# Kernel tuning notes

Measured on AMD Instinct MI355X. Metric: run time of the kernel, lower is better.

## Reference

```python
import jax, jax.numpy as jnp
import numpy as np

EPS = 1e-3  # BatchNorm eps (eval mode: running_mean=0, running_var=1)
GRID_D, GRID_H, GRID_W, GRID_C = 10, 400, 352, 128


def bn_last(x, g, b):
    # BatchNorm1d eval over last (channel) axis
    return x * (g / jnp.sqrt(1.0 + EPS)) + b


def bn_ch(x, g, b):
    # BatchNorm3d eval, channel axis 1 of NCDHW
    s = (g / jnp.sqrt(1.0 + EPS)).reshape(1, -1, 1, 1, 1)
    return x * s + b.reshape(1, -1, 1, 1, 1)


def vfe_layer(x, W, g, b):
    # x: [N, T, Cin] -> [N, T, 2*units]
    h = jnp.einsum('ntc,uc->ntu', x, W)
    h = jax.nn.relu(bn_last(h, g, b))
    agg = jnp.max(h, axis=1, keepdims=True)          # [N,1,units]
    return jnp.concatenate([h, jnp.broadcast_to(agg, h.shape)], axis=2)


def pad3(x, p):
    # torch ConstantPad3d order: (Wl, Wr, Hl, Hr, Dl, Dr); x is NCDHW
    return jnp.pad(x, ((0, 0), (0, 0), (p[4], p[5]), (p[2], p[3]), (p[0], p[1])))


def conv3d(x, w, stride):
    return jax.lax.conv_general_dilated(
        x, w, window_strides=stride, padding='VALID',
        dimension_numbers=('NCDHW', 'OIDHW', 'NCDHW'))


def setup_inputs() -> dict:
    key = jax.random.key(0)
    ks = jax.random.split(key, 12)
    N, T = 20000, 35
    features = jax.random.normal(ks[0], (N, T, 4), jnp.float32)
    num_voxels = jax.random.randint(ks[1], (N,), 1, T + 1, jnp.int32)
    cb = jnp.zeros((N, 1), jnp.int32)
    cd = jax.random.randint(ks[2], (N, 1), 0, GRID_D, jnp.int32)
    ch = jax.random.randint(ks[3], (N, 1), 0, GRID_H, jnp.int32)
    cw = jax.random.randint(ks[4], (N, 1), 0, GRID_W, jnp.int32)
    coors = jnp.concatenate([cb, cd, ch, cw], axis=1)

    def lin(k, o, i):
        return jax.random.normal(k, (o, i), jnp.float32) / np.sqrt(i)

    def cw3(k, o, i):
        return jax.random.normal(k, (o, i, 3, 3, 3), jnp.float32) / np.sqrt(i * 27)

    return {
        'features': features, 'num_voxels': num_voxels, 'coors': coors, 'batch_size': 1,
        'w_vfe1': lin(ks[5], 16, 7), 'g_vfe1': jnp.ones(16), 'b_vfe1': jnp.zeros(16),
        'w_vfe2': lin(ks[6], 64, 32), 'g_vfe2': jnp.ones(64), 'b_vfe2': jnp.zeros(64),
        'w_lin': lin(ks[7], 128, 128), 'g_lin': jnp.ones(128), 'b_lin': jnp.zeros(128),
        'w_c1': cw3(ks[8], 64, 128), 'g_c1': jnp.ones(64), 'b_c1': jnp.zeros(64),
        'w_c2': cw3(ks[9], 64, 64), 'g_c2': jnp.ones(64), 'b_c2': jnp.zeros(64),
        'w_c3': cw3(ks[10], 64, 64), 'g_c3': jnp.ones(64), 'b_c3': jnp.zeros(64),
    }


def reference(features, num_voxels, coors, batch_size,
              w_vfe1, g_vfe1, b_vfe1, w_vfe2, g_vfe2, b_vfe2,
              w_lin, g_lin, b_lin,
              w_c1, g_c1, b_c1, w_c2, g_c2, b_c2, w_c3, g_c3, b_c3):
    # --- VoxelFeatureExtractor ---
    nv = num_voxels.astype(features.dtype)[:, None, None]
    points_mean = features[:, :, :3].sum(axis=1, keepdims=True) / nv
    rel = features[:, :, :3] - points_mean
    f = jnp.concatenate([features, rel], axis=-1)                 # [N,T,7]
    T = f.shape[1]
    mask = (jnp.arange(T)[None, :] < num_voxels[:, None]).astype(f.dtype)[..., None]
    x = vfe_layer(f, w_vfe1, g_vfe1, b_vfe1) * mask               # [N,T,32]
    x = vfe_layer(x, w_vfe2, g_vfe2, b_vfe2) * mask               # [N,T,128]
    x = jnp.einsum('ntc,uc->ntu', x, w_lin)
    x = jax.nn.relu(bn_last(x, g_lin, b_lin)) * mask
    voxelwise = jnp.max(x, axis=1)                                # [N,128]

    # --- MiddleExtractor: scatter_nd + 3D convs ---
    grid = jnp.zeros((batch_size, GRID_D, GRID_H, GRID_W, GRID_C), f.dtype)
    grid = grid.at[coors[:, 0], coors[:, 1], coors[:, 2], coors[:, 3]].set(voxelwise)
    r = grid.transpose(0, 4, 1, 2, 3)                             # NCDHW [1,128,10,400,352]
    r = pad3(r, (1, 1, 1, 1, 1, 1))
    r = jax.nn.relu(bn_ch(conv3d(r, w_c1, (2, 1, 1)), g_c1, b_c1))  # [1,64,5,400,352]
    r = pad3(r, (1, 1, 1, 1, 0, 0))
    r = jax.nn.relu(bn_ch(conv3d(r, w_c2, (1, 1, 1)), g_c2, b_c2))  # [1,64,3,400,352]
    r = pad3(r, (1, 1, 1, 1, 1, 1))
    r = jax.nn.relu(bn_ch(conv3d(r, w_c3, (2, 1, 1)), g_c3, b_c3))  # [1,64,2,400,352]
    Nb, C, D, H, W = r.shape
    return r.reshape(Nb, C * D, H, W)                             # [1,128,400,352]
```

## Files before the change

kernel.cpp:

```cpp
#include <hip/hip_runtime.h>
#include <hip/hip_bf16.h>

#define BNC 0.99950037f
#define GH 400
#define GW 352

typedef __bf16 bf16_t;
typedef __bf16 bf16x8 __attribute__((ext_vector_type(8)));
typedef float f32x4 __attribute__((ext_vector_type(4)));

__global__ void k_winner(const int* __restrict__ coors, int* __restrict__ winner, int N) {
    int i = blockIdx.x * 256 + threadIdx.x;
    if (i >= N) return;
    int d = coors[i*4+1], h = coors[i*4+2], w = coors[i*4+3];
    atomicMax(&winner[(d*GH + h)*GW + w], i);
}

__global__ void k_tr_w(const float* __restrict__ w, float* __restrict__ wt, int CI, int CO) {
    int idx = blockIdx.x * 256 + threadIdx.x;
    int total = 27 * CI * CO;
    if (idx >= total) return;
    int j   = idx & 3;
    int t1  = idx >> 2;
    int co  = t1 % CO;
    int t2  = t1 / CO;
    int ci4 = t2 % (CI/4);
    int tap = t2 / (CI/4);
    int ci  = ci4*4 + j;
    wt[idx] = w[(co*CI + ci)*27 + tap];
}

__global__ void k_tr_lin(const float* __restrict__ wl, float* __restrict__ WT) {
    int idx = blockIdx.x * 256 + threadIdx.x;
    if (idx >= 16384) return;
    int u = idx & 127, c = idx >> 7;
    WT[c*128 + u] = wl[u*128 + c];
}

__global__ void k_prep(const float* __restrict__ g, const float* __restrict__ b,
                       float* __restrict__ out) {
    int i = threadIdx.x;
    if (i < 64)       out[i] = g[i] * BNC;
    else if (i < 128) out[i] = b[i-64];
    else if (i < 192) out[i] = 1.f;
    else              out[i] = 0.f;
}

__global__ void k_packw(const float* __restrict__ w, bf16_t* __restrict__ wh,
                        bf16_t* __restrict__ wlo) {
    int i = blockIdx.x * 256 + threadIdx.x;
    if (i >= 13824) return;
    int lane = i & 63, ct = (i >> 6) & 3, s = i >> 8;
    int tap = s >> 1, h = s & 1;
    int kg = lane >> 4, wl = lane & 15;
    int co = ct*16 + wl;
    #pragma unroll
    for (int j = 0; j < 8; ++j) {
        int ci = h*32 + kg*8 + j;
        float v = w[(co*64 + ci)*27 + tap];
        bf16_t hi = (bf16_t)v;
        wh[(long)i*8 + j]  = hi;
        wlo[(long)i*8 + j] = (bf16_t)(v - (float)hi);
    }
}

__global__ __launch_bounds__(128) void k_vfe(
    const float* __restrict__ feats, const int* __restrict__ nvox,
    const float* __restrict__ w1, const float* __restrict__ g1g, const float* __restrict__ b1g,
    const float* __restrict__ w2g, const float* __restrict__ g2g, const float* __restrict__ b2g,
    const float* __restrict__ WT, const float* __restrict__ glg, const float* __restrict__ blg,
    float* __restrict__ voxelwise)
{
    __shared__ float F[35*8];
    __shared__ float W1s[16*8];
    __shared__ float SG1[16], SB1[16];
    __shared__ float X1[35*20];
    __shared__ float X2[35*68];
    __shared__ float RED[8*128];
    __shared__ float AGG1[16];
    __shared__ float AGG2[64];
    __shared__ float Y2B[64];
    __shared__ float YB[128];
    __shared__ float MEANS[3];

    int tid = threadIdx.x;
    int vox = blockIdx.x;
    int nv  = nvox[vox];

    const float* fsrc = feats + (long)vox * 140;
    for (int idx = tid; idx < 140; idx += 128) { int t = idx>>2, c = idx&3; F[t*8+c] = fsrc[idx]; }
    if (tid < 35) F[tid*8+7] = 0.f;
    if (tid < 112) { int u = tid/7, c = tid - u*7; W1s[u*8+c] = w1[tid]; }
    if (tid < 16)  { W1s[tid*8+7] = 0.f; SG1[tid] = g1g[tid]*BNC; SB1[tid] = b1g[tid]; }
    __syncthreads();

    if (tid < 3) {
        float s = 0.f;
        for (int t = 0; t < 35; ++t) s += F[t*8 + tid];
        MEANS[tid] = s / (float)nv;
    }
    __syncthreads();
    for (int idx = tid; idx < 105; idx += 128) { int t = idx/3, c = idx - t*3; F[t*8+4+c] = F[t*8+c] - MEANS[c]; }
    __syncthreads();

    {
        const float4* Ff4  = (const float4*)F;
        const float4* W1f4 = (const float4*)W1s;
        for (int idx = tid; idx < 560; idx += 128) {
            int t = idx >> 4, u = idx & 15;
            float4 a0 = Ff4[t*2], a1 = Ff4[t*2+1];
            float4 b0 = W1f4[u*2], b1v = W1f4[u*2+1];
            float a = a0.x*b0.x + a0.y*b0.y + a0.z*b0.z + a0.w*b0.w
                    + a1.x*b1v.x + a1.y*b1v.y + a1.z*b1v.z + a1.w*b1v.w;
            X1[t*20+u] = fmaxf(a*SG1[u] + SB1[u], 0.f);
        }
    }
    __syncthreads();
    if (tid < 16) {
        float m = 0.f;
        for (int t = 0; t < 35; ++t) m = fmaxf(m, X1[t*20+tid]);
        AGG1[tid] = m;
    }
    __syncthreads();
    if (tid < 64) {
        const float4* wsrc = (const float4*)(w2g + tid*32 + 16);
        const float4* A1f4 = (const float4*)AGG1;
        float a = 0.f;
        #pragma unroll
        for (int q = 0; q < 4; ++q) {
            float4 w4 = wsrc[q], x4 = A1f4[q];
            a += x4.x*w4.x + x4.y*w4.y + x4.z*w4.z + x4.w*w4.w;
        }
        Y2B[tid] = a;
    }
    __syncthreads();

    {
        int u = tid & 63, tg = tid >> 6;
        float w2r[16];
        const float4* wsrc = (const float4*)(w2g + u*32);
        #pragma unroll
        for (int q = 0; q < 4; ++q) {
            float4 w4 = wsrc[q];
            w2r[q*4] = w4.x; w2r[q*4+1] = w4.y; w2r[q*4+2] = w4.z; w2r[q*4+3] = w4.w;
        }
        float su = g2g[u]*BNC, bu = b2g[u];
        float yb2 = Y2B[u];
        float lm = (nv < 35) ? fmaxf(bu, 0.f) : 0.f;
        for (int t = tg; t < nv; t += 2) {
            const float4* xr = (const float4*)(X1 + t*20);
            float a = yb2;
            #pragma unroll
            for (int q = 0; q < 4; ++q) {
                float4 x4 = xr[q];
                a += x4.x*w2r[q*4] + x4.y*w2r[q*4+1] + x4.z*w2r[q*4+2] + x4.w*w2r[q*4+3];
            }
            float h = fmaxf(a*su + bu, 0.f);
            X2[t*68 + u] = h;
            lm = fmaxf(lm, h);
        }
        RED[tg*64 + u] = lm;
    }
    __syncthreads();
    if (tid < 64) AGG2[tid] = fmaxf(RED[tid], RED[64+tid]);
    __syncthreads();
    {
        float a = 0.f;
        for (int c = 0; c < 64; ++c) a = fmaf(AGG2[c], WT[(64 + c)*128 + tid], a);
        YB[tid] = a;
    }
    __syncthreads();

    {
        int ug = tid & 15, tg4 = tid >> 4;
        int u0 = ug * 8;
        int kmax = (nv > tg4) ? ((nv - tg4 + 7) >> 3) : 0;
        float acc[5][8];
        #pragma unroll
        for (int k = 0; k < 5; ++k)
            #pragma unroll
            for (int j = 0; j < 8; ++j) acc[k][j] = 0.f;

        const float4* X2f4 = (const float4*)X2;
        const float4* WTf4 = (const float4*)WT;
        for (int c4 = 0; c4 < 16; ++c4) {
            float4 wv[8];
            #pragma unroll
            for (int cc = 0; cc < 4; ++cc) {
                wv[cc*2]   = WTf4[(c4*4+cc)*32 + ug*2];
                wv[cc*2+1] = WTf4[(c4*4+cc)*32 + ug*2 + 1];
            }
            #pragma unroll
            for (int k = 0; k < 5; ++k) {
                if (k < kmax) {
                    int t = tg4 + (k << 3);
                    float4 x4 = X2f4[t*17 + c4];
                    #pragma unroll
                    for (int cc = 0; cc < 4; ++cc) {
                        float xs = (cc == 0) ? x4.x : (cc == 1) ? x4.y : (cc == 2) ? x4.z : x4.w;
                        acc[k][0] = fmaf(xs, wv[cc*2].x,   acc[k][0]);
                        acc[k][1] = fmaf(xs, wv[cc*2].y,   acc[k][1]);
                        acc[k][2] = fmaf(xs, wv[cc*2].z,   acc[k][2]);
                        acc[k][3] = fmaf(xs, wv[cc*2].w,   acc[k][3]);
                        acc[k][4] = fmaf(xs, wv[cc*2+1].x, acc[k][4]);
                        acc[k][5] = fmaf(xs, wv[cc*2+1].y, acc[k][5]);
                        acc[k][6] = fmaf(xs, wv[cc*2+1].z, acc[k][6]);
                        acc[k][7] = fmaf(xs, wv[cc*2+1].w, acc[k][7]);
                    }
                }
            }
        }
        float4 g0 = *(const float4*)(glg + u0), g1v = *(const float4*)(glg + u0 + 4);
        float4 b0 = *(const float4*)(blg + u0), b1v = *(const float4*)(blg + u0 + 4);
        float4 y0 = *(const float4*)(YB + u0),  y1v = *(const float4*)(YB + u0 + 4);
        float sg[8] = {g0.x*BNC, g0.y*BNC, g0.z*BNC, g0.w*BNC,
                       g1v.x*BNC, g1v.y*BNC, g1v.z*BNC, g1v.w*BNC};
        float sb[8] = {b0.x, b0.y, b0.z, b0.w, b1v.x, b1v.y, b1v.z, b1v.w};
        float yv[8] = {y0.x, y0.y, y0.z, y0.w, y1v.x, y1v.y, y1v.z, y1v.w};
        float m[8];
        #pragma unroll
        for (int j = 0; j < 8; ++j) m[j] = 0.f;
        #pragma unroll
        for (int k = 0; k < 5; ++k) {
            if (k < kmax) {
                #pragma unroll
                for (int j = 0; j < 8; ++j)
                    m[j] = fmaxf(m[j], fmaxf((acc[k][j] + yv[j])*sg[j] + sb[j], 0.f));
            }
        }
        #pragma unroll
        for (int j = 0; j < 8; ++j) RED[tg4*128 + u0 + j] = m[j];
    }
    __syncthreads();
    {
        float m = RED[tid];
        #pragma unroll
        for (int r = 1; r < 8; ++r) m = fmaxf(m, RED[r*128 + tid]);
        voxelwise[(long)vox*128 + tid] = m;
    }
}

__global__ __launch_bounds__(256) void k_gat1(
    const float4* __restrict__ voxf4, const int* __restrict__ winner,
    const float4* __restrict__ Wt1, float* __restrict__ accS,
    int h_lo, int AR)
{
    int r  = blockIdx.y;
    int oh = h_lo + r;
    if ((unsigned)oh >= (unsigned)GH) return;
    int doo = blockIdx.z;
    int w0  = blockIdx.x * 32;

    __shared__ int sList[306];
    __shared__ int sCnt;
    __shared__ float4 sF[32][32];

    int t = threadIdx.x;
    if (t == 0) sCnt = 0;
    __syncthreads();
    for (int idx = t; idx < 306; idx += 256) {
        int x = idx % 34, q = idx / 34;
        int kd = q / 3, kh = q - kd*3;
        int dp = doo*2 + kd - 1;
        int hp = oh + kh - 1;
        int wp = w0 - 1 + x;
        if ((unsigned)dp < 10u && (unsigned)hp < (unsigned)GH && (unsigned)wp < (unsigned)GW) {
            int v = winner[(dp*GH + hp)*GW + wp];
            if (v >= 0) {
                int p = atomicAdd(&sCnt, 1);
                sList[p] = (v << 10) | (kd << 8) | (kh << 6) | x;
            }
        }
    }
    __syncthreads();
    int cnt = sCnt;

    int co = t & 63, wv = t >> 6;
    int ibase = wv*8;
    float acc[8];
    #pragma unroll
    for (int i = 0; i < 8; ++i) acc[i] = 0.f;

    for (int c0 = 0; c0 < cnt; c0 += 32) {
        int nch = min(32, cnt - c0);
        __syncthreads();
        for (int idx = t; idx < nch*32; idx += 256) {
            int slot = idx >> 5, c = idx & 31;
            int widx = sList[c0 + slot] >> 10;
            sF[slot][c] = voxf4[(long)widx*32 + c];
        }
        __syncthreads();
        for (int e = 0; e < nch; ++e) {
            int ent = sList[c0 + e];
            int x = ent & 63, kh = (ent >> 6) & 3, kd = (ent >> 8) & 3;
            #pragma unroll
            for (int kw = 0; kw < 3; ++kw) {
                int i = x - kw;
                if (i >= ibase && i < ibase + 8) {
                    const float4* wb = Wt1 + (long)(kd*9 + kh*3 + kw)*2048 + co;
                    float a = 0.f;
                    #pragma unroll 4
                    for (int c4 = 0; c4 < 32; ++c4) {
                        float4 wq = wb[c4*64];
                        float4 f4 = sF[e][c4];
                        a += f4.x*wq.x + f4.y*wq.y + f4.z*wq.z + f4.w*wq.w;
                    }
                    int j = i - ibase;
                    #pragma unroll
                    for (int j8 = 0; j8 < 8; ++j8)
                        if (j8 == j) acc[j8] += a;
                }
            }
        }
    }

    long rowb = ((long)doo*AR + r)*GW + w0;
    #pragma unroll
    for (int i = 0; i < 8; ++i)
        accS[(rowb + ibase + i)*64 + co] = acc[i];
}

__global__ __launch_bounds__(256) void k_convm(
    const float* __restrict__ src, int src_h0, long src_dpitch,
    float* __restrict__ dst, int dst_h0, long sC, long sD, long sH, long sW,
    const bf16_t* __restrict__ wph, const bf16_t* __restrict__ wpl,
    const float* __restrict__ gact,
    const float* __restrict__ gout, const float* __restrict__ bout,
    int D_in, int d_stride, int d_pad, int y0)
{
    int oh = y0 + (int)blockIdx.y;
    if ((unsigned)oh >= (unsigned)GH) return;

    __shared__ __align__(16) char smem[17408];
    bf16_t* sAh = (bf16_t*)smem;
    bf16_t* sAl = (bf16_t*)(smem + 8448);
    float*  sOut = (float*)smem;

    int t = threadIdx.x;
    int lane = t & 63, wv = t >> 6;
    int wl = lane & 15, kg = lane >> 4;
    int mh = wv >> 1, cth = wv & 1;
    int w0 = (int)blockIdx.x * 64;
    int od = (int)blockIdx.z;

    f32x4 acc[2][2];
    #pragma unroll
    for (int a = 0; a < 2; ++a)
        #pragma unroll
        for (int b = 0; b < 2; ++b) acc[a][b] = (f32x4){0.f, 0.f, 0.f, 0.f};

    const bf16x8* WH = (const bf16x8*)wph;
    const bf16x8* WL = (const bf16x8*)wpl;

    for (int kd = 0; kd < 3; ++kd) {
        int dp = od*d_stride + kd - d_pad;
        if (dp < 0 || dp >= D_in) continue;
        const float* sdb = src + dp*src_dpitch;
        for (int kh = 0; kh < 3; ++kh) {
            int hp = oh + kh - 1;
            bool vh = ((unsigned)hp < (unsigned)GH);
            const float* srow = sdb + (long)(hp - src_h0) * (GW*64);
            __syncthreads();
            for (int c = t; c < 528; c += 256) {
                int g = c & 7, w = c >> 3;
                int gw = w0 - 1 + w;
                f32x4 v0 = {0.f,0.f,0.f,0.f}, v1 = {0.f,0.f,0.f,0.f};
                if (vh && (unsigned)gw < (unsigned)GW) {
                    const float* p = srow + (long)gw*64 + g*8;
                    v0 = *(const f32x4*)p;
                    v1 = *(const f32x4*)(p + 4);
                    f32x4 ga = *(const f32x4*)(gact + g*8);
                    f32x4 gb = *(const f32x4*)(gact + g*8 + 4);
                    f32x4 ba = *(const f32x4*)(gact + 64 + g*8);
                    f32x4 bb = *(const f32x4*)(gact + 64 + g*8 + 4);
                    #pragma unroll
                    for (int e = 0; e < 4; ++e) {
                        v0[e] = fmaxf(v0[e]*ga[e] + ba[e], 0.f);
                        v1[e] = fmaxf(v1[e]*gb[e] + bb[e], 0.f);
                    }
                }
                bf16x8 hi, lo;
                #pragma unroll
                for (int e = 0; e < 4; ++e) {
                    bf16_t h0 = (bf16_t)v0[e];
                    hi[e] = h0; lo[e] = (bf16_t)(v0[e] - (float)h0);
                    bf16_t h1 = (bf16_t)v1[e];
                    hi[4+e] = h1; lo[4+e] = (bf16_t)(v1[e] - (float)h1);
                }
                *(bf16x8*)&sAh[(g*66 + w)*8] = hi;
                *(bf16x8*)&sAl[(g*66 + w)*8] = lo;
            }
            __syncthreads();
            #pragma unroll
            for (int h = 0; h < 2; ++h) {
                #pragma unroll
                for (int kw = 0; kw < 3; ++kw) {
                    int s = ((kd*3 + kh)*3 + kw)*2 + h;
                    long fb = (long)(s*4 + cth*2)*64 + lane;
                    bf16x8 B0h = WH[fb],      B0l = WL[fb];
                    bf16x8 B1h = WH[fb + 64], B1l = WL[fb + 64];
                    #pragma unroll
                    for (int mt = 0; mt < 2; ++mt) {
                        int ai = ((h*4 + kg)*66 + (mh*2 + mt)*16 + kw + wl)*8;
                        bf16x8 Ah = *(const bf16x8*)&sAh[ai];
                        bf16x8 Al = *(const bf16x8*)&sAl[ai];
                        acc[mt][0] = __builtin_amdgcn_mfma_f32_16x16x32_bf16(Ah, B0h, acc[mt][0], 0, 0, 0);
                        acc[mt][0] = __builtin_amdgcn_mfma_f32_16x16x32_bf16(Ah, B0l, acc[mt][0], 0, 0, 0);
                        acc[mt][0] = __builtin_amdgcn_mfma_f32_16x16x32_bf16(Al, B0h, acc[mt][0], 0, 0, 0);
                        acc[mt][1] = __builtin_amdgcn_mfma_f32_16x16x32_bf16(Ah, B1h, acc[mt][1], 0, 0, 0);
                        acc[mt][1] = __builtin_amdgcn_mfma_f32_16x16x32_bf16(Ah, B1l, acc[mt][1], 0, 0, 0);
                        acc[mt][1] = __builtin_amdgcn_mfma_f32_16x16x32_bf16(Al, B1h, acc[mt][1], 0, 0, 0);
                    }
                }
            }
        }
    }

    float so[2], bo[2];
    #pragma unroll
    for (int ct = 0; ct < 2; ++ct) {
        int co = (cth*2 + ct)*16 + wl;
        so[ct] = gout[co]*BNC; bo[ct] = bout[co];
    }
    if (sW == 1) {
        #pragma unroll
        for (int mt = 0; mt < 2; ++mt) {
            int ow = w0 + (mh*2 + mt)*16 + kg*4;
            if (ow < GW) {
                #pragma unroll
                for (int ct = 0; ct < 2; ++ct) {
                    int co = (cth*2 + ct)*16 + wl;
                    f32x4 r;
                    #pragma unroll
                    for (int e = 0; e < 4; ++e)
                        r[e] = fmaxf(acc[mt][ct][e]*so[ct] + bo[ct], 0.f);
                    *(f32x4*)&dst[(long)co*sC + (long)od*sD + (long)(oh - dst_h0)*sH + ow] = r;
                }
            }
        }
    } else {
        __syncthreads();
        #pragma unroll
        for (int mt = 0; mt < 2; ++mt)
            #pragma unroll
            for (int ct = 0; ct < 2; ++ct) {
                int co = (cth*2 + ct)*16 + wl;
                #pragma unroll
                for (int e = 0; e < 4; ++e) {
                    int owl = (mh*2 + mt)*16 + kg*4 + e;
                    sOut[owl*68 + co] = fmaxf(acc[mt][ct][e]*so[ct] + bo[ct], 0.f);
                }
            }
        __syncthreads();
        for (int f = t; f < 1024; f += 256) {
            int w = f >> 4, c4 = f & 15;
            if (w0 + w < GW) {
                float4 v = *(const float4*)&sOut[w*68 + c4*4];
                *(float4*)&dst[(long)od*sD + (long)(oh - dst_h0)*sH + (long)(w0 + w)*64 + c4*4] = v;
            }
        }
    }
}

extern "C" void kernel_launch(void* const* d_in, const int* in_sizes, int n_in,
                              void* d_out, int out_size, void* d_ws, size_t ws_size,
                              hipStream_t stream)
{
    const float* feats = (const float*)d_in[0];
    const int*   nvox  = (const int*)d_in[1];
    const int*   coors = (const int*)d_in[2];
    const float* w1  = (const float*)d_in[4];
    const float* g1  = (const float*)d_in[5];
    const float* b1  = (const float*)d_in[6];
    const float* w2  = (const float*)d_in[7];
    const float* g2  = (const float*)d_in[8];
    const float* b2  = (const float*)d_in[9];
    const float* wl  = (const float*)d_in[10];
    const float* gl  = (const float*)d_in[11];
    const float* bl  = (const float*)d_in[12];
    const float* wc1 = (const float*)d_in[13];
    const float* gc1 = (const float*)d_in[14];
    const float* bc1 = (const float*)d_in[15];
    const float* wc2 = (const float*)d_in[16];
    const float* gc2 = (const float*)d_in[17];
    const float* bc2 = (const float*)d_in[18];
    const float* wc3 = (const float*)d_in[19];
    const float* gc3 = (const float*)d_in[20];
    const float* bc3 = (const float*)d_in[21];

    int N = in_sizes[1];

    auto al = [](size_t b) { return (b + 255) & ~(size_t)255; };

    size_t winB = al((size_t)10*GH*GW*4);
    size_t voxB = al((size_t)N*128*4);
    size_t w1B  = al((size_t)27*128*64*4);
    size_t wlB  = al((size_t)128*128*4);
    size_t wpB  = al((size_t)13824*8*2);
    int NS = 20;
    const int cand[8] = {1, 2, 4, 5, 8, 10, 16, 20};
    for (int k = 0; k < 8; ++k) {
        int ns = cand[k], sh = 400/ns, ar = sh + 4, xr = sh + 2;
        size_t tot = al((size_t)5*ar*GW*64*4) + al((size_t)3*xr*GW*64*4)
                   + winB + voxB + w1B + wlB + 4*wpB + 4096;
        if (tot + (1<<16) <= ws_size) { NS = ns; break; }
    }
    int SH = 400/NS, AR = SH + 4, XR = SH + 2;

    char* ws = (char*)d_ws;
    size_t off = 0;
    auto alloc = [&](size_t bytes) -> void* {
        void* p = ws + off; off += al(bytes); return p;
    };
    size_t accB = (size_t)5*AR*GW*64*4;
    size_t actB = (size_t)3*XR*GW*64*4;
    float*  accS   = (float*)alloc(accB);
    float*  actS   = (float*)alloc(actB);
    int*    winner = (int*)alloc((size_t)10*GH*GW*4);
    float*  voxw   = (float*)alloc((size_t)N*128*4);
    float*  wt1    = (float*)alloc((size_t)27*128*64*4);
    float*  wtl    = (float*)alloc((size_t)128*128*4);
    bf16_t* wp2h   = (bf16_t*)alloc(wpB);
    bf16_t* wp2l   = (bf16_t*)alloc(wpB);
    bf16_t* wp3h   = (bf16_t*)alloc(wpB);
    bf16_t* wp3l   = (bf16_t*)alloc(wpB);
    float*  gact   = (float*)alloc(256*4);

    hipMemsetAsync(winner, 0xFF, (size_t)10*GH*GW*4, stream);

    k_tr_w<<<(27*128*64 + 255)/256, 256, 0, stream>>>(wc1, wt1, 128, 64);
    k_tr_lin<<<64, 256, 0, stream>>>(wl, wtl);
    k_packw<<<54, 256, 0, stream>>>(wc2, wp2h, wp2l);
    k_packw<<<54, 256, 0, stream>>>(wc3, wp3h, wp3l);
    k_prep<<<1, 256, 0, stream>>>(gc1, bc1, gact);

    k_winner<<<(N + 255)/256, 256, 0, stream>>>(coors, winner, N);
    k_vfe<<<N, 128, 0, stream>>>(feats, nvox, w1, g1, b1, w2, g2, b2, wtl, gl, bl, voxw);

    for (int s = 0; s < NS; ++s) {
        k_gat1<<<dim3(11, AR, 5), 256, 0, stream>>>(
            (const float4*)voxw, winner, (const float4*)wt1,
            accS, s*SH - 2, AR);
        k_convm<<<dim3(6, SH + 2, 3), 256, 0, stream>>>(
            accS, s*SH - 2, (long)AR*GW*64,
            actS, s*SH - 1, 1L, (long)XR*GW*64, (long)GW*64, 64L,
            wp2h, wp2l, gact, gc2, bc2,
            5, 1, 0, s*SH - 1);
        k_convm<<<dim3(6, SH, 2), 256, 0, stream>>>(
            actS, s*SH - 1, (long)XR*GW*64,
            (float*)d_out, 0, (long)2*GH*GW, (long)GH*GW, (long)GW, 1L,
            wp3h, wp3l, gact + 128, gc3, bc3,
            3, 2, 1, s*SH);
    }
}
```

Measured before the change: 1.015 ms.

## Store intermediate activations pre-split as bf16 hi/lo planes and pack two voxels per VFE block

The first conv's BN+ReLU and the bf16 hi/lo split move into the producer kernels. The intermediate grids are now stored as two bf16 planes instead of fp32, so the conv kernels load bf16x8 directly without per-load activation and conversion math. Separately, the VFE kernel processes two voxels per 256-thread block using per-voxel shared-memory slices. This cuts the per-element conversion work repeated across the 9 taps in each conv. The trade-off is more staging iterations in the tile loader and extra bf16 plane writes.

```diff
diff --git a/kernel.cpp b/kernel.cpp
--- a/kernel.cpp
+++ b/kernel.cpp
@@ -7,6 +7,7 @@
 
 typedef __bf16 bf16_t;
 typedef __bf16 bf16x8 __attribute__((ext_vector_type(8)));
+typedef __bf16 bf16x4 __attribute__((ext_vector_type(4)));
 typedef float f32x4 __attribute__((ext_vector_type(4)));
 
 __global__ void k_winner(const int* __restrict__ coors, int* __restrict__ winner, int N) {
@@ -42,8 +43,6 @@
     int i = threadIdx.x;
     if (i < 64)       out[i] = g[i] * BNC;
     else if (i < 128) out[i] = b[i-64];
-    else if (i < 192) out[i] = 1.f;
-    else              out[i] = 0.f;
 }
 
 __global__ void k_packw(const float* __restrict__ w, bf16_t* __restrict__ wh,
@@ -64,49 +63,53 @@
     }
 }
 
-__global__ __launch_bounds__(128) void k_vfe(
+__global__ __launch_bounds__(256) void k_vfe(
     const float* __restrict__ feats, const int* __restrict__ nvox,
     const float* __restrict__ w1, const float* __restrict__ g1g, const float* __restrict__ b1g,
     const float* __restrict__ w2g, const float* __restrict__ g2g, const float* __restrict__ b2g,
     const float* __restrict__ WT, const float* __restrict__ glg, const float* __restrict__ blg,
-    float* __restrict__ voxelwise)
+    float* __restrict__ voxelwise, int N)
 {
-    __shared__ float F[35*8];
+    __shared__ float S[2][4672];
     __shared__ float W1s[16*8];
     __shared__ float SG1[16], SB1[16];
-    __shared__ float X1[35*20];
-    __shared__ float X2[35*68];
-    __shared__ float RED[8*128];
-    __shared__ float AGG1[16];
-    __shared__ float AGG2[64];
-    __shared__ float Y2B[64];
-    __shared__ float YB[128];
-    __shared__ float MEANS[3];
 
     int tid = threadIdx.x;
-    int vox = blockIdx.x;
+    int v   = tid >> 7, lt = tid & 127;
+    int vox = blockIdx.x*2 + v;
+    if (vox >= N) vox = N - 1;
     int nv  = nvox[vox];
 
+    float* F     = &S[v][0];
+    float* X1    = &S[v][280];
+    float* X2    = &S[v][980];
+    float* RED   = &S[v][3360];
+    float* AGG1  = &S[v][4384];
+    float* AGG2  = &S[v][4400];
+    float* Y2B   = &S[v][4464];
+    float* YB    = &S[v][4528];
+    float* MEANS = &S[v][4656];
+
     const float* fsrc = feats + (long)vox * 140;
-    for (int idx = tid; idx < 140; idx += 128) { int t = idx>>2, c = idx&3; F[t*8+c] = fsrc[idx]; }
-    if (tid < 35) F[tid*8+7] = 0.f;
+    for (int idx = lt; idx < 140; idx += 128) { int t = idx>>2, c = idx&3; F[t*8+c] = fsrc[idx]; }
+    if (lt < 35) F[lt*8+7] = 0.f;
     if (tid < 112) { int u = tid/7, c = tid - u*7; W1s[u*8+c] = w1[tid]; }
     if (tid < 16)  { W1s[tid*8+7] = 0.f; SG1[tid] = g1g[tid]*BNC; SB1[tid] = b1g[tid]; }
     __syncthreads();
 
-    if (tid < 3) {
+    if (lt < 3) {
         float s = 0.f;
-        for (int t = 0; t < 35; ++t) s += F[t*8 + tid];
-        MEANS[tid] = s / (float)nv;
-    }
-    __syncthreads();
-    for (int idx = tid; idx < 105; idx += 128) { int t = idx/3, c = idx - t*3; F[t*8+4+c] = F[t*8+c] - MEANS[c]; }
+        for (int t = 0; t < 35; ++t) s += F[t*8 + lt];
+        MEANS[lt] = s / (float)nv;
+    }
+    __syncthreads();
+    for (int idx = lt; idx < 105; idx += 128) { int t = idx/3, c = idx - t*3; F[t*8+4+c] = F[t*8+c] - MEANS[c]; }
     __syncthreads();
 
     {
         const float4* Ff4  = (const float4*)F;
         const float4* W1f4 = (const float4*)W1s;
-        for (int idx = tid; idx < 560; idx += 128) {
+        for (int idx = lt; idx < 560; idx += 128) {
             int t = idx >> 4, u = idx & 15;
             float4 a0 = Ff4[t*2], a1 = Ff4[t*2+1];
             float4 b0 = W1f4[u*2], b1v = W1f4[u*2+1];
@@ -116,14 +119,14 @@
         }
     }
     __syncthreads();
-    if (tid < 16) {
+    if (lt < 16) {
         float m = 0.f;
-        for (int t = 0; t < 35; ++t) m = fmaxf(m, X1[t*20+tid]);
-        AGG1[tid] = m;
-    }
-    __syncthreads();
-    if (tid < 64) {
-        const float4* wsrc = (const float4*)(w2g + tid*32 + 16);
+        for (int t = 0; t < 35; ++t) m = fmaxf(m, X1[t*20+lt]);
+        AGG1[lt] = m;
+    }
+    __syncthreads();
+    if (lt < 64) {
+        const float4* wsrc = (const float4*)(w2g + lt*32 + 16);
         const float4* A1f4 = (const float4*)AGG1;
         float a = 0.f;
         #pragma unroll
@@ -131,12 +134,12 @@
             float4 w4 = wsrc[q], x4 = A1f4[q];
             a += x4.x*w4.x + x4.y*w4.y + x4.z*w4.z + x4.w*w4.w;
         }
-        Y2B[tid] = a;
+        Y2B[lt] = a;
     }
     __syncthreads();
 
     {
-        int u = tid & 63, tg = tid >> 6;
+        int u = lt & 63, tg = lt >> 6;
         float w2r[16];
         const float4* wsrc = (const float4*)(w2g + u*32);
         #pragma unroll
@@ -162,17 +165,17 @@
         RED[tg*64 + u] = lm;
     }
     __syncthreads();
-    if (tid < 64) AGG2[tid] = fmaxf(RED[tid], RED[64+tid]);
+    if (lt < 64) AGG2[lt] = fmaxf(RED[lt], RED[64+lt]);
     __syncthreads();
     {
         float a = 0.f;
-        for (int c = 0; c < 64; ++c) a = fmaf(AGG2[c], WT[(64 + c)*128 + tid], a);
-        YB[tid] = a;
+        for (int c = 0; c < 64; ++c) a = fmaf(AGG2[c], WT[(64 + c)*128 + lt], a);
+        YB[lt] = a;
     }
     __syncthreads();
 
     {
-        int ug = tid & 15, tg4 = tid >> 4;
+        int ug = lt & 15, tg4 = lt >> 4;
         int u0 = ug * 8;
         int kmax = (nv > tg4) ? ((nv - tg4 + 7) >> 3) : 0;
         float acc[5][8];
@@ -233,16 +236,17 @@
     }
     __syncthreads();
     {
-        float m = RED[tid];
-        #pragma unroll
-        for (int r = 1; r < 8; ++r) m = fmaxf(m, RED[r*128 + tid]);
-        voxelwise[(long)vox*128 + tid] = m;
+        float m = RED[lt];
+        #pragma unroll
+        for (int r = 1; r < 8; ++r) m = fmaxf(m, RED[r*128 + lt]);
+        voxelwise[(long)vox*128 + lt] = m;
     }
 }
 
 __global__ __launch_bounds__(256) void k_gat1(
     const float4* __restrict__ voxf4, const int* __restrict__ winner,
-    const float4* __restrict__ Wt1, float* __restrict__ accS,
+    const float4* __restrict__ Wt1, bf16_t* __restrict__ accH,
+    bf16_t* __restrict__ accL, const float* __restrict__ gact,
     int h_lo, int AR)
 {
     int r  = blockIdx.y;
@@ -314,17 +318,24 @@
         }
     }
 
+    float g = gact[co], b = gact[64 + co];
     long rowb = ((long)doo*AR + r)*GW + w0;
     #pragma unroll
-    for (int i = 0; i < 8; ++i)
-        accS[(rowb + ibase + i)*64 + co] = acc[i];
+    for (int i = 0; i < 8; ++i) {
+        float rr = fmaxf(acc[i]*g + b, 0.f);
+        bf16_t hi = (bf16_t)rr;
+        long idx = (rowb + ibase + i)*64 + co;
+        accH[idx] = hi;
+        accL[idx] = (bf16_t)(rr - (float)hi);
+    }
 }
 
 __global__ __launch_bounds__(256) void k_convm(
-    const float* __restrict__ src, int src_h0, long src_dpitch,
-    float* __restrict__ dst, int dst_h0, long sC, long sD, long sH, long sW,
+    const bf16_t* __restrict__ srcH, const bf16_t* __restrict__ srcL,
+    int src_h0, long src_dpitch,
+    float* __restrict__ dstF, bf16_t* __restrict__ dstH, bf16_t* __restrict__ dstL,
+    int dst_h0, long sC, long sD, long sH,
     const bf16_t* __restrict__ wph, const bf16_t* __restrict__ wpl,
-    const float* __restrict__ gact,
     const float* __restrict__ gout, const float* __restrict__ bout,
     int D_in, int d_stride, int d_pad, int y0)
 {
@@ -355,40 +366,28 @@
     for (int kd = 0; kd < 3; ++kd) {
         int dp = od*d_stride + kd - d_pad;
         if (dp < 0 || dp >= D_in) continue;
-        const float* sdb = src + dp*src_dpitch;
+        const bf16_t* sdbH = srcH + dp*src_dpitch;
+        const bf16_t* sdbL = srcL + dp*src_dpitch;
         for (int kh = 0; kh < 3; ++kh) {
             int hp = oh + kh - 1;
             bool vh = ((unsigned)hp < (unsigned)GH);
-            const float* srow = sdb + (long)(hp - src_h0) * (GW*64);
+            long rowoff = (long)(hp - src_h0) * (GW*64);
             __syncthreads();
-            for (int c = t; c < 528; c += 256) {
-                int g = c & 7, w = c >> 3;
+            for (int c = t; c < 1056; c += 256) {
+                int pl = (c >= 528) ? 1 : 0;
+                int cc = c - (pl << 9) - (pl << 4);
+                int g = cc / 66, w = cc - g*66;
                 int gw = w0 - 1 + w;
-                f32x4 v0 = {0.f,0.f,0.f,0.f}, v1 = {0.f,0.f,0.f,0.f};
+                bf16x8 vv;
                 if (vh && (unsigned)gw < (unsigned)GW) {
-                    const float* p = srow + (long)gw*64 + g*8;
-                    v0 = *(const f32x4*)p;
-                    v1 = *(const f32x4*)(p + 4);
-                    f32x4 ga = *(const f32x4*)(gact + g*8);
-                    f32x4 gb = *(const f32x4*)(gact + g*8 + 4);
-                    f32x4 ba = *(const f32x4*)(gact + 64 + g*8);
-                    f32x4 bb = *(const f32x4*)(gact + 64 + g*8 + 4);
+                    const bf16_t* plane = pl ? sdbL : sdbH;
+                    vv = *(const bf16x8*)(plane + rowoff + (long)gw*64 + g*8);
+                } else {
                     #pragma unroll
-                    for (int e = 0; e < 4; ++e) {
-                        v0[e] = fmaxf(v0[e]*ga[e] + ba[e], 0.f);
-                        v1[e] = fmaxf(v1[e]*gb[e] + bb[e], 0.f);
-                    }
+                    for (int e = 0; e < 8; ++e) vv[e] = (bf16_t)0.f;
                 }
-                bf16x8 hi, lo;
-                #pragma unroll
-                for (int e = 0; e < 4; ++e) {
-                    bf16_t h0 = (bf16_t)v0[e];
-                    hi[e] = h0; lo[e] = (bf16_t)(v0[e] - (float)h0);
-                    bf16_t h1 = (bf16_t)v1[e];
-                    hi[4+e] = h1; lo[4+e] = (bf16_t)(v1[e] - (float)h1);
-                }
-                *(bf16x8*)&sAh[(g*66 + w)*8] = hi;
-                *(bf16x8*)&sAl[(g*66 + w)*8] = lo;
+                bf16_t* dstl = pl ? sAl : sAh;
+                *(bf16x8*)&dstl[(g*66 + w)*8] = vv;
             }
             __syncthreads();
             #pragma unroll
@@ -422,7 +421,7 @@
         int co = (cth*2 + ct)*16 + wl;
         so[ct] = gout[co]*BNC; bo[ct] = bout[co];
     }
-    if (sW == 1) {
+    if (dstF) {
         #pragma unroll
         for (int mt = 0; mt < 2; ++mt) {
             int ow = w0 + (mh*2 + mt)*16 + kg*4;
@@ -434,7 +433,7 @@
                     #pragma unroll
                     for (int e = 0; e < 4; ++e)
                         r[e] = fmaxf(acc[mt][ct][e]*so[ct] + bo[ct], 0.f);
-                    *(f32x4*)&dst[(long)co*sC + (long)od*sD + (long)(oh - dst_h0)*sH + ow] = r;
+                    *(f32x4*)&dstF[(long)co*sC + (long)od*sD + (long)(oh - dst_h0)*sH + ow] = r;
                 }
             }
         }
@@ -456,7 +455,14 @@
             int w = f >> 4, c4 = f & 15;
             if (w0 + w < GW) {
                 float4 v = *(const float4*)&sOut[w*68 + c4*4];
-                *(float4*)&dst[(long)od*sD + (long)(oh - dst_h0)*sH + (long)(w0 + w)*64 + c4*4] = v;
+                long base = (long)od*sD + (long)(oh - dst_h0)*sH + (long)(w0 + w)*64 + c4*4;
+                bf16_t h0 = (bf16_t)v.x, h1 = (bf16_t)v.y, h2 = (bf16_t)v.z, h3 = (bf16_t)v.w;
+                bf16x4 hv; hv[0]=h0; hv[1]=h1; hv[2]=h2; hv[3]=h3;
+                bf16x4 lv;
+                lv[0]=(bf16_t)(v.x-(float)h0); lv[1]=(bf16_t)(v.y-(float)h1);
+                lv[2]=(bf16_t)(v.z-(float)h2); lv[3]=(bf16_t)(v.w-(float)h3);
+                *(bf16x4*)&dstH[base] = hv;
+                *(bf16x4*)&dstL[base] = lv;
             }
         }
     }
@@ -501,7 +507,7 @@
     const int cand[8] = {1, 2, 4, 5, 8, 10, 16, 20};
     for (int k = 0; k < 8; ++k) {
         int ns = cand[k], sh = 400/ns, ar = sh + 4, xr = sh + 2;
-        size_t tot = al((size_t)5*ar*GW*64*4) + al((size_t)3*xr*GW*64*4)
+        size_t tot = 2*al((size_t)5*ar*GW*64*2) + 2*al((size_t)3*xr*GW*64*2)
                    + winB + voxB + w1B + wlB + 4*wpB + 4096;
         if (tot + (1<<16) <= ws_size) { NS = ns; break; }
     }
@@ -512,10 +518,12 @@
     auto alloc = [&](size_t bytes) -> void* {
         void* p = ws + off; off += al(bytes); return p;
     };
-    size_t accB = (size_t)5*AR*GW*64*4;
-    size_t actB = (size_t)3*XR*GW*64*4;
-    float*  accS   = (float*)alloc(accB);
-    float*  actS   = (float*)alloc(actB);
+    size_t accB = (size_t)5*AR*GW*64*2;
+    size_t actB = (size_t)3*XR*GW*64*2;
+    bf16_t* accH   = (bf16_t*)alloc(accB);
+    bf16_t* accL   = (bf16_t*)alloc(accB);
+    bf16_t* actH   = (bf16_t*)alloc(actB);
+    bf16_t* actL   = (bf16_t*)alloc(actB);
     int*    winner = (int*)alloc((size_t)10*GH*GW*4);
     float*  voxw   = (float*)alloc((size_t)N*128*4);
     float*  wt1    = (float*)alloc((size_t)27*128*64*4);
@@ -535,21 +543,22 @@
     k_prep<<<1, 256, 0, stream>>>(gc1, bc1, gact);
 
     k_winner<<<(N + 255)/256, 256, 0, stream>>>(coors, winner, N);
-    k_vfe<<<N, 128, 0, stream>>>(feats, nvox, w1, g1, b1, w2, g2, b2, wtl, gl, bl, voxw);
+    k_vfe<<<(N + 1)/2, 256, 0, stream>>>(feats, nvox, w1, g1, b1, w2, g2, b2,
+                                         wtl, gl, bl, voxw, N);
 
     for (int s = 0; s < NS; ++s) {
         k_gat1<<<dim3(11, AR, 5), 256, 0, stream>>>(
             (const float4*)voxw, winner, (const float4*)wt1,
-            accS, s*SH - 2, AR);
+            accH, accL, gact, s*SH - 2, AR);
         k_convm<<<dim3(6, SH + 2, 3), 256, 0, stream>>>(
-            accS, s*SH - 2, (long)AR*GW*64,
-            actS, s*SH - 1, 1L, (long)XR*GW*64, (long)GW*64, 64L,
-            wp2h, wp2l, gact, gc2, bc2,
+            accH, accL, s*SH - 2, (long)AR*GW*64,
+            nullptr, actH, actL, s*SH - 1, 0L, (long)XR*GW*64, (long)GW*64,
+            wp2h, wp2l, gc2, bc2,
             5, 1, 0, s*SH - 1);
         k_convm<<<dim3(6, SH, 2), 256, 0, stream>>>(
-            actS, s*SH - 1, (long)XR*GW*64,
-            (float*)d_out, 0, (long)2*GH*GW, (long)GH*GW, (long)GW, 1L,
-            wp3h, wp3l, gact + 128, gc3, bc3,
+            actH, actL, s*SH - 1, (long)XR*GW*64,
+            (float*)d_out, nullptr, nullptr, 0, (long)2*GH*GW, (long)GH*GW, (long)GW,
+            wp3h, wp3l, gc3, bc3,
             3, 2, 1, s*SH);
     }
 }
```

Result: slower. 1.083 ms (+6.7%).
